# Kernel tuning notes

Measured on AMD Instinct MI355X. Metric: run time of the kernel, lower is better.

The kernel has to match this reference:

```python
import jax, jax.numpy as jnp
import numpy as np

H = 16            # num_heads
D = 64            # head_output_size
DIM = 1024        # model dim (C)
R = 10            # lora rank
ATT_SCALE = D ** -0.5
LORA_SCALE = 1.0 / R   # lora_alpha(=1) / r


def setup_inputs() -> dict:
    key = jax.random.key(0)
    ks = jax.random.split(key, 14)
    B, N = 2, 2048
    s = 0.02
    x = jax.random.normal(ks[0], (B, N, DIM), jnp.float32)
    mask = jax.random.randint(ks[1], (B, N), 0, 2).astype(bool)
    return {
        "x": x,
        "mask": mask,
        "w_qkv": jax.random.normal(ks[2], (3 * H * D, DIM), jnp.float32) * s,
        "wq_base": jax.random.normal(ks[3], (H * D, DIM), jnp.float32) * s,
        "bq_base": jax.random.normal(ks[4], (H * D,), jnp.float32) * s,
        "wq_A": jax.random.normal(ks[5], (R, DIM), jnp.float32) * s,
        "wq_B": jax.random.normal(ks[6], (H * D, R), jnp.float32) * s,
        "wv_base": jax.random.normal(ks[7], (H * D, DIM), jnp.float32) * s,
        "bv_base": jax.random.normal(ks[8], (H * D,), jnp.float32) * s,
        "wv_A": jax.random.normal(ks[9], (R, DIM), jnp.float32) * s,
        "wv_B": jax.random.normal(ks[10], (H * D, R), jnp.float32) * s,
        "w_out": jax.random.normal(ks[11], (DIM, H * D), jnp.float32) * s,
        "b_out": jax.random.normal(ks[12], (DIM,), jnp.float32) * s,
    }


def _lora_linear(x, w_base, b_base, A, Bm):
    # lora.Linear (unmerged): base linear + scaled low-rank path
    return x @ w_base.T + b_base + ((x @ A.T) @ Bm.T) * LORA_SCALE


def reference(x, mask, w_qkv, wq_base, bq_base, wq_A, wq_B,
              wv_base, bv_base, wv_A, wv_B, w_out, b_out):
    B, N, C = x.shape
    # fused qkv projection -> (3, B, H, N, D)
    qkv = (x @ w_qkv.T).reshape(B, N, 3, H, D).transpose(2, 0, 3, 1, 4)
    q, k, v = qkv[0], qkv[1], qkv[2]
    # LoRA-modified q and v, reshaped to (B, H, N, D)
    q_lora = _lora_linear(x, wq_base, bq_base, wq_A, wq_B).reshape(B, N, H, D).transpose(0, 2, 1, 3)
    v_lora = _lora_linear(x, wv_base, bv_base, wv_A, wv_B).reshape(B, N, H, D).transpose(0, 2, 1, 3)
    q = q + q_lora
    v = v + v_lora
    # attention scores (B, H, N, N)
    attn = jnp.einsum('bhnd,bhmd->bhnm', q, k) * ATT_SCALE
    # 2D key-padding mask branch: mask[:, None, None, :]
    attn = jnp.where(mask[:, None, None, :], attn, -jnp.inf)
    attn = jax.nn.softmax(attn, axis=-1)
    out = jnp.einsum('bhnm,bhmd->bhnd', attn, v)
    out = out.transpose(0, 2, 1, 3).reshape(B, N, H * D)  # b h n d -> b n (h d)
    return out @ w_out.T + b_out
```

## Files before the change

### kernel.cpp

```cpp
#include <hip/hip_runtime.h>

typedef unsigned short u16;
typedef unsigned int u32;
typedef __attribute__((ext_vector_type(2))) unsigned int u32x2;
typedef __attribute__((ext_vector_type(4))) unsigned int u32x4;
typedef __attribute__((ext_vector_type(4))) unsigned short u16x4;
typedef __attribute__((ext_vector_type(8))) unsigned short u16x8;
typedef __attribute__((ext_vector_type(8))) short short8;
typedef __attribute__((ext_vector_type(4))) float f32x4;
typedef __attribute__((ext_vector_type(16))) float f32x16;

#define NHEAD 16
#define HDIM 64
#define SEQ 2048
#define MODELD 1024
#define MROWS 4096
#define QKVCOLS 3072
#define QSCALE 0.18033688011112042f

#define WAITVM(N) asm volatile("s_waitcnt vmcnt(" #N ")" ::: "memory")

__device__ __forceinline__ u16 f2bf(float f) {
  union { float f; unsigned u; } v; v.f = f;
  unsigned r = v.u + 0x7FFFu + ((v.u >> 16) & 1u);
  return (u16)(r >> 16);
}

__device__ __forceinline__ u32 cvtpk(float lo, float hi) {
  u32 r;
  asm("v_cvt_pk_bf16_f32 %0, %1, %2" : "=v"(r) : "v"(lo), "v"(hi));
  return r;
}

__device__ __forceinline__ void pl32(u32& a, u32& b) {
  asm("v_permlane32_swap_b32 %0, %1" : "+v"(a), "+v"(b));
}

__device__ __forceinline__ void gload_lds16(const void* g, void* l) {
  __builtin_amdgcn_global_load_lds((const __attribute__((address_space(1))) void*)g,
                                   (__attribute__((address_space(3))) void*)l, 16, 0, 0);
}


__global__ void prep_cast(const float* __restrict__ in, u16* __restrict__ outb) {
  int i = blockIdx.x * 256 + threadIdx.x;
  float4 v = *(const float4*)(in + (size_t)i * 4);
  u16x4 o = {f2bf(v.x), f2bf(v.y), f2bf(v.z), f2bf(v.w)};
  *(u16x4*)(outb + (size_t)i * 4) = o;
}

__global__ void prep_mask(const unsigned int* __restrict__ mraw, u16* __restrict__ mbf) {
  __shared__ int flag;
  const int tid = threadIdx.x;
  if (tid == 0) flag = 0;
  __syncthreads();
  if (mraw[tid] > 1u) flag = 1;
  __syncthreads();
  const int is_bytes = flag;
  const unsigned char* bp = (const unsigned char*)mraw;
  u16x4 o;
#pragma unroll
  for (int j = 0; j < 4; ++j) {
    unsigned v = is_bytes ? (unsigned)bp[tid * 4 + j] : mraw[tid * 4 + j];
    o[j] = v ? (u16)0 : (u16)0xC380;
  }
  *(u16x4*)(mbf + tid * 4) = o;
}

__global__ void prep_w(const float* __restrict__ wqkv,
                       const float* __restrict__ wqb, const float* __restrict__ bq,
                       const float* __restrict__ wqA, const float* __restrict__ wqB,
                       const float* __restrict__ wvb, const float* __restrict__ bv,
                       const float* __restrict__ wvA, const float* __restrict__ wvB,
                       u16* __restrict__ wcomb, float* __restrict__ biasc) {
  const int c = blockIdx.x;
  const int t = c >> 10, hd = c & 1023;
  const int k0 = threadIdx.x * 4;
  float4 w = *(const float4*)(wqkv + (size_t)c * MODELD + k0);
  float a0 = w.x, a1 = w.y, a2 = w.z, a3 = w.w;
  if (t != 1) {
    const float* base = (t == 0 ? wqb : wvb) + (size_t)hd * MODELD + k0;
    const float* A = (t == 0 ? wqA : wvA);
    const float* Bm = (t == 0 ? wqB : wvB) + hd * 10;
    float4 bsv = *(const float4*)base;
    a0 += bsv.x; a1 += bsv.y; a2 += bsv.z; a3 += bsv.w;
#pragma unroll
    for (int j = 0; j < 10; ++j) {
      float bj = Bm[j] * 0.1f;
      float4 av = *(const float4*)(A + (size_t)j * MODELD + k0);
      a0 += bj * av.x; a1 += bj * av.y; a2 += bj * av.z; a3 += bj * av.w;
    }
    if (t == 0) { a0 *= QSCALE; a1 *= QSCALE; a2 *= QSCALE; a3 *= QSCALE; }
  }
  u16x4 o = {f2bf(a0), f2bf(a1), f2bf(a2), f2bf(a3)};
  *(u16x4*)(wcomb + (size_t)c * MODELD + k0) = o;
  if (threadIdx.x == 0)
    biasc[c] = (t == 0) ? QSCALE * bq[hd] : ((t == 2) ? bv[hd] : 0.f);
}

template<int MODE>
__global__ __launch_bounds__(256) void gemm128(const u16* __restrict__ A, const u16* __restrict__ W,
                                               const float* __restrict__ bias,
                                               u16* __restrict__ oq, u16* __restrict__ ok, u16* __restrict__ ov,
                                               float* __restrict__ of) {
  __shared__ __align__(16) char lds[65536];
  const int tid = threadIdx.x;
  const int lane = tid & 63;
  const int wid = tid >> 6;
  const int wr = wid >> 1, wc = wid & 1;
  const int nx = gridDim.x;
  int bid = blockIdx.y * nx + blockIdx.x;
  bid = (bid & 7) * ((nx * gridDim.y) >> 3) + (bid >> 3);
  const int m0 = (bid / nx) << 7;
  const int n0 = (bid % nx) << 7;
  const int K = MODELD;

  f32x4 acc[4][4] = {};
  const int so = wid * 1024 + (lane << 4);

  auto stage = [&](int buf, int kt) {
    char* dst = lds + (buf << 15);
#pragma unroll
    for (int c = 0; c < 4; ++c) {
      const int o = c * 4096 + so;
      const int row = o >> 7;
      const int colb = (o & 127) ^ ((row & 7) << 4);
      gload_lds16((const char*)(A + (size_t)(m0 + row) * K + kt) + colb, dst + (c * 4096 + wid * 1024));
      gload_lds16((const char*)(W + (size_t)(n0 + row) * K + kt) + colb, dst + (16384 + c * 4096 + wid * 1024));
    }
  };

  stage(0, 0);
  __syncthreads();

  for (int t = 0; t < 16; ++t) {
    if (t < 15) stage((t + 1) & 1, (t + 1) << 6);
    const char* base = lds + ((t & 1) << 15);
#pragma unroll
    for (int ks = 0; ks < 2; ++ks) {
      short8 av[4], bv[4];
#pragma unroll
      for (int i = 0; i < 4; ++i) {
        const int arow = wr * 64 + i * 16 + (lane & 15);
        const int off = (ks * 64 + ((lane >> 4) << 4)) ^ ((lane & 7) << 4);
        av[i] = *(const short8*)(base + (arow << 7) + off);
        const int brow = wc * 64 + i * 16 + (lane & 15);
        bv[i] = *(const short8*)(base + 16384 + (brow << 7) + off);
      }
#pragma unroll
      for (int i = 0; i < 4; ++i)
#pragma unroll
        for (int j = 0; j < 4; ++j)
          acc[i][j] = __builtin_amdgcn_mfma_f32_16x16x32_bf16(av[i], bv[j], acc[i][j], 0, 0, 0);
    }
    __syncthreads();
  }

  if (MODE == 0) {
    u16* limg = (u16*)lds;
    const int tsel = n0 >> 10;
    const int hd0 = n0 & 1023;
#pragma unroll
    for (int j = 0; j < 4; ++j) {
      const int cl = wc * 64 + j * 16 + (lane & 15);
      const int head = cl >> 6, d = cl & 63;
      const float bs = bias[n0 + cl];
#pragma unroll
      for (int i = 0; i < 4; ++i) {
        const int kvb = wr * 64 + i * 16 + ((lane >> 4) << 2);
#pragma unroll
        for (int r = 0; r < 4; ++r) {
          const int kvloc = kvb + r;
          const u16 val = f2bf(acc[i][j][r] + bs);
          int off;
          if (tsel == 0) {
            off = head * 8192 + kvloc * 64 + d;
          } else if (tsel == 1) {
            const int kv = kvloc & 63;
            off = head * 8192 + (kvloc >> 6) * 4096 +
                  ((((kv >> 5) & 1) << 2) + (d >> 4)) * 512 +
                  (((kv & 31) + (((d >> 3) & 1) << 5)) << 3) + (d & 7);
          } else {
            const int kv = kvloc & 63;
            off = head * 8192 + (kvloc >> 6) * 4096 +
                  (((d >> 5) << 2) + ((kv >> 4) & 3)) * 512 +
                  (((d & 31) + (((kv >> 3) & 1) << 5)) << 3) + (kv & 7);
          }
          limg[off] = val;
        }
      }
    }
    __syncthreads();
    const int b = m0 >> 11;
#pragma unroll
    for (int p = 0; p < 8; ++p) {
      const int idx = p * 2048 + tid * 8;
      u16x8 v = *(const u16x8*)(limg + idx);
      const int headg = (hd0 >> 6) + (p >> 2);
      const size_t bh = (size_t)(b * NHEAD + headg);
      if (tsel == 0) {
        u16* dst = oq + (bh * SEQ + (m0 & 2047)) * HDIM + (p & 3) * 2048 + tid * 8;
        *(u16x8*)dst = v;
      } else {
        const int tileg = ((m0 & 2047) >> 6) + ((p >> 1) & 1);
        u16* basep = (tsel == 1) ? ok : ov;
        u16* dst = basep + (bh * 32 + tileg) * 4096 + (p & 1) * 2048 + tid * 8;
        *(u16x8*)dst = v;
      }
    }
  } else {
#pragma unroll
    for (int j = 0; j < 4; ++j) {
      const int col = n0 + wc * 64 + j * 16 + (lane & 15);
      const float bs = bias[col];
#pragma unroll
      for (int i = 0; i < 4; ++i) {
        const int rowb = m0 + wr * 64 + i * 16 + ((lane >> 4) << 2);
#pragma unroll
        for (int r = 0; r < 4; ++r)
          of[(size_t)(rowb + r) * MODELD + col] = acc[i][j][r] + bs;
      }
    }
  }
}

__global__ __launch_bounds__(64, 2) void flash_attn(const u16* __restrict__ q, const u16* __restrict__ kfr,
                                                    const u16* __restrict__ vfr, const u16* __restrict__ mbf,
                                                    u16* __restrict__ attnout) {
  const int lane = threadIdx.x;
  const int qi = lane & 31, h = lane >> 5;
  const int bid = blockIdx.x;
  const int xcd = bid & 7, rest = bid >> 3;
  const int bh = xcd * 4 + (rest >> 6);
  const int q0 = (rest & 63) << 5;
  const int b = bh >> 4, hh = bh & 15;

  const int token = q0 + qi;
  short8 qf[4], qf4 = {};
  {
    const u16* qp = q + ((size_t)bh * SEQ + token) * HDIM;
#pragma unroll
    for (int ks = 0; ks < 4; ++ks) qf[ks] = *(const short8*)(qp + ks * 16 + h * 8);
    if (h == 0) qf4[0] = (short)0x3F80;
  }

  const u16* kg = kfr + (size_t)bh * 32 * 4096;
  const u16* vg = vfr + (size_t)bh * 32 * 4096;
  const u16* mrow = mbf + b * SEQ;
  const int lo = lane << 3;

  short8 kS[8], vS[8];
  u16 m0v, m1v;

  f32x16 o0 = {}, o1 = {};
  f32x4 ps = {0.f, 0.f, 0.f, 0.f};

  {
    const u16* kt = kg;
    const u16* vt = vg;
#pragma unroll
    for (int i = 0; i < 8; ++i) kS[i] = *(const short8*)(kt + i * 512 + lo);
#pragma unroll
    for (int i = 0; i < 8; ++i) vS[i] = *(const short8*)(vt + i * 512 + lo);
    m0v = mrow[qi];
    m1v = mrow[32 + qi];
  }

  for (int t = 0; t < 32; ++t) {
    short8 e0 = {}, e1 = {};
    if (h == 0) { e0[0] = (short)m0v; e1[0] = (short)m1v; }

    f32x16 s0 = {}, s1 = {};
    __builtin_amdgcn_s_setprio(1);
#pragma unroll
    for (int ks = 0; ks < 4; ++ks) {
      s0 = __builtin_amdgcn_mfma_f32_32x32x16_bf16(kS[ks], qf[ks], s0, 0, 0, 0);
      s1 = __builtin_amdgcn_mfma_f32_32x32x16_bf16(kS[4 + ks], qf[ks], s1, 0, 0, 0);
    }
    s0 = __builtin_amdgcn_mfma_f32_32x32x16_bf16(e0, qf4, s0, 0, 0, 0);
    s1 = __builtin_amdgcn_mfma_f32_32x32x16_bf16(e1, qf4, s1, 0, 0, 0);
    __builtin_amdgcn_s_setprio(0);

    if (t < 31) {
      const u16* kt = kg + (size_t)(t + 1) * 4096;
#pragma unroll
      for (int i = 0; i < 8; ++i) kS[i] = *(const short8*)(kt + i * 512 + lo);
      m0v = mrow[(t + 1) * 64 + qi];
      m1v = mrow[(t + 1) * 64 + 32 + qi];
    }

    u32 w[16];
#pragma unroll
    for (int blk = 0; blk < 2; ++blk) {
#pragma unroll
      for (int g = 0; g < 4; ++g) {
        float e0f, e1f, e2f, e3f;
        if (blk == 0) {
          e0f = __builtin_amdgcn_exp2f(s0[4 * g + 0]);
          e1f = __builtin_amdgcn_exp2f(s0[4 * g + 1]);
          e2f = __builtin_amdgcn_exp2f(s0[4 * g + 2]);
          e3f = __builtin_amdgcn_exp2f(s0[4 * g + 3]);
        } else {
          e0f = __builtin_amdgcn_exp2f(s1[4 * g + 0]);
          e1f = __builtin_amdgcn_exp2f(s1[4 * g + 1]);
          e2f = __builtin_amdgcn_exp2f(s1[4 * g + 2]);
          e3f = __builtin_amdgcn_exp2f(s1[4 * g + 3]);
        }
        ps[0] += e0f; ps[1] += e1f; ps[2] += e2f; ps[3] += e3f;
        w[blk * 8 + 2 * g] = cvtpk(e0f, e1f);
        w[blk * 8 + 2 * g + 1] = cvtpk(e2f, e3f);
      }
    }
    pl32(w[0], w[2]);  pl32(w[1], w[3]);
    pl32(w[4], w[6]);  pl32(w[5], w[7]);
    pl32(w[8], w[10]); pl32(w[9], w[11]);
    pl32(w[12], w[14]); pl32(w[13], w[15]);

    __builtin_amdgcn_s_setprio(1);
#pragma unroll
    for (int s = 0; s < 4; ++s) {
      u32x4 pw = {w[4 * s], w[4 * s + 1], w[4 * s + 2], w[4 * s + 3]};
      short8 pf = __builtin_bit_cast(short8, pw);
      o0 = __builtin_amdgcn_mfma_f32_32x32x16_bf16(vS[s], pf, o0, 0, 0, 0);
      o1 = __builtin_amdgcn_mfma_f32_32x32x16_bf16(vS[4 + s], pf, o1, 0, 0, 0);
    }
    __builtin_amdgcn_s_setprio(0);

    if (t < 31) {
      const u16* vt = vg + (size_t)(t + 1) * 4096;
#pragma unroll
      for (int i = 0; i < 8; ++i) vS[i] = *(const short8*)(vt + i * 512 + lo);
    }
  }

  float l = (ps[0] + ps[1]) + (ps[2] + ps[3]);
  l += __shfl_xor(l, 32);
  const float inv = 1.0f / l;

  u16* outp = attnout + ((size_t)(b * SEQ + token)) * MODELD + hh * HDIM;
#pragma unroll
  for (int dblk = 0; dblk < 2; ++dblk) {
#pragma unroll
    for (int g = 0; g < 4; ++g) {
      float v0, v1, v2, v3;
      if (dblk == 0) {
        v0 = o0[4 * g + 0]; v1 = o0[4 * g + 1]; v2 = o0[4 * g + 2]; v3 = o0[4 * g + 3];
      } else {
        v0 = o1[4 * g + 0]; v1 = o1[4 * g + 1]; v2 = o1[4 * g + 2]; v3 = o1[4 * g + 3];
      }
      u32x2 ow;
      ow[0] = cvtpk(v0 * inv, v1 * inv);
      ow[1] = cvtpk(v2 * inv, v3 * inv);
      *(u32x2*)(outp + dblk * 32 + g * 8 + h * 4) = ow;
    }
  }
}

extern "C" void kernel_launch(void* const* d_in, const int* in_sizes, int n_in,
                              void* d_out, int out_size, void* d_ws, size_t ws_size,
                              hipStream_t stream) {
  const float* x       = (const float*)d_in[0];
  const unsigned int* mask = (const unsigned int*)d_in[1];
  const float* w_qkv   = (const float*)d_in[2];
  const float* wq_base = (const float*)d_in[3];
  const float* bq      = (const float*)d_in[4];
  const float* wq_A    = (const float*)d_in[5];
  const float* wq_B    = (const float*)d_in[6];
  const float* wv_base = (const float*)d_in[7];
  const float* bv      = (const float*)d_in[8];
  const float* wv_A    = (const float*)d_in[9];
  const float* wv_B    = (const float*)d_in[10];
  const float* w_out   = (const float*)d_in[11];
  const float* b_out   = (const float*)d_in[12];
  float* out = (float*)d_out;

  char* ws = (char*)d_ws;
  u16* xb      = (u16*)(ws);
  u16* wcomb   = (u16*)(ws + 8388608);
  u16* woutb   = (u16*)(ws + 14680064);
  u16* qws     = (u16*)(ws + 16777216);
  u16* kws     = (u16*)(ws + 25165824);
  u16* vws     = (u16*)(ws + 33554432);
  float* biasc = (float*)(ws + 50331648);
  u16* mbf     = (u16*)(ws + 50343936);
  u16* attnout = xb;

  prep_cast<<<4096, 256, 0, stream>>>(x, xb);
  prep_cast<<<1024, 256, 0, stream>>>(w_out, woutb);
  prep_mask<<<1, 1024, 0, stream>>>(mask, mbf);
  prep_w<<<3072, 256, 0, stream>>>(w_qkv, wq_base, bq, wq_A, wq_B,
                                   wv_base, bv, wv_A, wv_B, wcomb, biasc);

  gemm128<0><<<dim3(QKVCOLS / 128, MROWS / 128), 256, 0, stream>>>(
      xb, wcomb, biasc, qws, kws, vws, nullptr);

  flash_attn<<<2048, 64, 0, stream>>>(qws, kws, vws, mbf, attnout);

  gemm128<1><<<dim3(MODELD / 128, MROWS / 128), 256, 0, stream>>>(
      attnout, woutb, b_out, nullptr, nullptr, nullptr, out);
}
```

Measured before the change: 138.8 us.

## Process two 32-query tiles per attention wave to reuse K/V fragments

Each flash-attention wave now handles 64 queries as two 32-query sub-tiles, both sharing the same K and V register fragments loaded once per key block. The grid is halved and the block-to-(head, query) mapping is adjusted to match. This cuts K/V global loads per query in half and gives the second tile's MFMAs time to hide the next K load. In exchange it needs more registers, since the launch-bounds occupancy hint was dropped and four output accumulators are live, and there are fewer waves to spread across CUs.

Result: no change. 137.7 us (-0.8%).

```diff
diff --git a/kernel.cpp b/kernel.cpp
--- a/kernel.cpp
+++ b/kernel.cpp
@@ -17,8 +17,6 @@
 #define MROWS 4096
 #define QKVCOLS 3072
 #define QSCALE 0.18033688011112042f
-
-#define WAITVM(N) asm volatile("s_waitcnt vmcnt(" #N ")" ::: "memory")
 
 __device__ __forceinline__ u16 f2bf(float f) {
   union { float f; unsigned u; } v; v.f = f;
@@ -224,23 +222,26 @@
   }
 }
 
-__global__ __launch_bounds__(64, 2) void flash_attn(const u16* __restrict__ q, const u16* __restrict__ kfr,
-                                                    const u16* __restrict__ vfr, const u16* __restrict__ mbf,
-                                                    u16* __restrict__ attnout) {
+__global__ __launch_bounds__(64) void flash_attn(const u16* __restrict__ q, const u16* __restrict__ kfr,
+                                                 const u16* __restrict__ vfr, const u16* __restrict__ mbf,
+                                                 u16* __restrict__ attnout) {
   const int lane = threadIdx.x;
   const int qi = lane & 31, h = lane >> 5;
   const int bid = blockIdx.x;
   const int xcd = bid & 7, rest = bid >> 3;
-  const int bh = xcd * 4 + (rest >> 6);
-  const int q0 = (rest & 63) << 5;
+  const int bh = xcd * 4 + (rest >> 5);
+  const int q0 = (rest & 31) << 6;
   const int b = bh >> 4, hh = bh & 15;
 
-  const int token = q0 + qi;
-  short8 qf[4], qf4 = {};
+  const int tokenA = q0 + qi;
+  short8 qfA[4], qfB[4], qf4 = {};
   {
-    const u16* qp = q + ((size_t)bh * SEQ + token) * HDIM;
-#pragma unroll
-    for (int ks = 0; ks < 4; ++ks) qf[ks] = *(const short8*)(qp + ks * 16 + h * 8);
+    const u16* qp = q + ((size_t)bh * SEQ + tokenA) * HDIM;
+#pragma unroll
+    for (int ks = 0; ks < 4; ++ks) {
+      qfA[ks] = *(const short8*)(qp + ks * 16 + h * 8);
+      qfB[ks] = *(const short8*)(qp + 32 * HDIM + ks * 16 + h * 8);
+    }
     if (h == 0) qf4[0] = (short)0x3F80;
   }
 
@@ -252,16 +253,14 @@
   short8 kS[8], vS[8];
   u16 m0v, m1v;
 
-  f32x16 o0 = {}, o1 = {};
-  f32x4 ps = {0.f, 0.f, 0.f, 0.f};
+  f32x16 oA0 = {}, oA1 = {}, oB0 = {}, oB1 = {};
+  f32x4 psA = {0.f, 0.f, 0.f, 0.f}, psB = {0.f, 0.f, 0.f, 0.f};
 
   {
-    const u16* kt = kg;
-    const u16* vt = vg;
-#pragma unroll
-    for (int i = 0; i < 8; ++i) kS[i] = *(const short8*)(kt + i * 512 + lo);
-#pragma unroll
-    for (int i = 0; i < 8; ++i) vS[i] = *(const short8*)(vt + i * 512 + lo);
+#pragma unroll
+    for (int i = 0; i < 8; ++i) kS[i] = *(const short8*)(kg + i * 512 + lo);
+#pragma unroll
+    for (int i = 0; i < 8; ++i) vS[i] = *(const short8*)(vg + i * 512 + lo);
     m0v = mrow[qi];
     m1v = mrow[32 + qi];
   }
@@ -274,20 +273,12 @@
     __builtin_amdgcn_s_setprio(1);
 #pragma unroll
     for (int ks = 0; ks < 4; ++ks) {
-      s0 = __builtin_amdgcn_mfma_f32_32x32x16_bf16(kS[ks], qf[ks], s0, 0, 0, 0);
-      s1 = __builtin_amdgcn_mfma_f32_32x32x16_bf16(kS[4 + ks], qf[ks], s1, 0, 0, 0);
+      s0 = __builtin_amdgcn_mfma_f32_32x32x16_bf16(kS[ks], qfA[ks], s0, 0, 0, 0);
+      s1 = __builtin_amdgcn_mfma_f32_32x32x16_bf16(kS[4 + ks], qfA[ks], s1, 0, 0, 0);
     }
     s0 = __builtin_amdgcn_mfma_f32_32x32x16_bf16(e0, qf4, s0, 0, 0, 0);
     s1 = __builtin_amdgcn_mfma_f32_32x32x16_bf16(e1, qf4, s1, 0, 0, 0);
     __builtin_amdgcn_s_setprio(0);
-
-    if (t < 31) {
-      const u16* kt = kg + (size_t)(t + 1) * 4096;
-#pragma unroll
-      for (int i = 0; i < 8; ++i) kS[i] = *(const short8*)(kt + i * 512 + lo);
-      m0v = mrow[(t + 1) * 64 + qi];
-      m1v = mrow[(t + 1) * 64 + 32 + qi];
-    }
 
     u32 w[16];
 #pragma unroll
@@ -306,7 +297,7 @@
           e2f = __builtin_amdgcn_exp2f(s1[4 * g + 2]);
           e3f = __builtin_amdgcn_exp2f(s1[4 * g + 3]);
         }
-        ps[0] += e0f; ps[1] += e1f; ps[2] += e2f; ps[3] += e3f;
+        psA[0] += e0f; psA[1] += e1f; psA[2] += e2f; psA[3] += e3f;
         w[blk * 8 + 2 * g] = cvtpk(e0f, e1f);
         w[blk * 8 + 2 * g + 1] = cvtpk(e2f, e3f);
       }
@@ -321,8 +312,61 @@
     for (int s = 0; s < 4; ++s) {
       u32x4 pw = {w[4 * s], w[4 * s + 1], w[4 * s + 2], w[4 * s + 3]};
       short8 pf = __builtin_bit_cast(short8, pw);
-      o0 = __builtin_amdgcn_mfma_f32_32x32x16_bf16(vS[s], pf, o0, 0, 0, 0);
-      o1 = __builtin_amdgcn_mfma_f32_32x32x16_bf16(vS[4 + s], pf, o1, 0, 0, 0);
+      oA0 = __builtin_amdgcn_mfma_f32_32x32x16_bf16(vS[s], pf, oA0, 0, 0, 0);
+      oA1 = __builtin_amdgcn_mfma_f32_32x32x16_bf16(vS[4 + s], pf, oA1, 0, 0, 0);
+    }
+
+    f32x16 r0 = {}, r1 = {};
+#pragma unroll
+    for (int ks = 0; ks < 4; ++ks) {
+      r0 = __builtin_amdgcn_mfma_f32_32x32x16_bf16(kS[ks], qfB[ks], r0, 0, 0, 0);
+      r1 = __builtin_amdgcn_mfma_f32_32x32x16_bf16(kS[4 + ks], qfB[ks], r1, 0, 0, 0);
+    }
+    r0 = __builtin_amdgcn_mfma_f32_32x32x16_bf16(e0, qf4, r0, 0, 0, 0);
+    r1 = __builtin_amdgcn_mfma_f32_32x32x16_bf16(e1, qf4, r1, 0, 0, 0);
+    __builtin_amdgcn_s_setprio(0);
+
+    if (t < 31) {
+      const u16* kt = kg + (size_t)(t + 1) * 4096;
+#pragma unroll
+      for (int i = 0; i < 8; ++i) kS[i] = *(const short8*)(kt + i * 512 + lo);
+      m0v = mrow[(t + 1) * 64 + qi];
+      m1v = mrow[(t + 1) * 64 + 32 + qi];
+    }
+
+#pragma unroll
+    for (int blk = 0; blk < 2; ++blk) {
+#pragma unroll
+      for (int g = 0; g < 4; ++g) {
+        float e0f, e1f, e2f, e3f;
+        if (blk == 0) {
+          e0f = __builtin_amdgcn_exp2f(r0[4 * g + 0]);
+          e1f = __builtin_amdgcn_exp2f(r0[4 * g + 1]);
+          e2f = __builtin_amdgcn_exp2f(r0[4 * g + 2]);
+          e3f = __builtin_amdgcn_exp2f(r0[4 * g + 3]);
+        } else {
+          e0f = __builtin_amdgcn_exp2f(r1[4 * g + 0]);
+          e1f = __builtin_amdgcn_exp2f(r1[4 * g + 1]);
+          e2f = __builtin_amdgcn_exp2f(r1[4 * g + 2]);
+          e3f = __builtin_amdgcn_exp2f(r1[4 * g + 3]);
+        }
+        psB[0] += e0f; psB[1] += e1f; psB[2] += e2f; psB[3] += e3f;
+        w[blk * 8 + 2 * g] = cvtpk(e0f, e1f);
+        w[blk * 8 + 2 * g + 1] = cvtpk(e2f, e3f);
+      }
+    }
+    pl32(w[0], w[2]);  pl32(w[1], w[3]);
+    pl32(w[4], w[6]);  pl32(w[5], w[7]);
+    pl32(w[8], w[10]); pl32(w[9], w[11]);
+    pl32(w[12], w[14]); pl32(w[13], w[15]);
+
+    __builtin_amdgcn_s_setprio(1);
+#pragma unroll
+    for (int s = 0; s < 4; ++s) {
+      u32x4 pw = {w[4 * s], w[4 * s + 1], w[4 * s + 2], w[4 * s + 3]};
+      short8 pf = __builtin_bit_cast(short8, pw);
+      oB0 = __builtin_amdgcn_mfma_f32_32x32x16_bf16(vS[s], pf, oB0, 0, 0, 0);
+      oB1 = __builtin_amdgcn_mfma_f32_32x32x16_bf16(vS[4 + s], pf, oB1, 0, 0, 0);
     }
     __builtin_amdgcn_s_setprio(0);
 
@@ -333,25 +377,33 @@
     }
   }
 
-  float l = (ps[0] + ps[1]) + (ps[2] + ps[3]);
-  l += __shfl_xor(l, 32);
-  const float inv = 1.0f / l;
-
-  u16* outp = attnout + ((size_t)(b * SEQ + token)) * MODELD + hh * HDIM;
+  float lA = (psA[0] + psA[1]) + (psA[2] + psA[3]);
+  lA += __shfl_xor(lA, 32);
+  float lB = (psB[0] + psB[1]) + (psB[2] + psB[3]);
+  lB += __shfl_xor(lB, 32);
+  const float invA = 1.0f / lA, invB = 1.0f / lB;
+
+  u16* outp = attnout + ((size_t)(b * SEQ + tokenA)) * MODELD + hh * HDIM;
 #pragma unroll
   for (int dblk = 0; dblk < 2; ++dblk) {
 #pragma unroll
     for (int g = 0; g < 4; ++g) {
-      float v0, v1, v2, v3;
+      float a0, a1, a2, a3, b0, b1, b2, b3;
       if (dblk == 0) {
-        v0 = o0[4 * g + 0]; v1 = o0[4 * g + 1]; v2 = o0[4 * g + 2]; v3 = o0[4 * g + 3];
+        a0 = oA0[4 * g + 0]; a1 = oA0[4 * g + 1]; a2 = oA0[4 * g + 2]; a3 = oA0[4 * g + 3];
+        b0 = oB0[4 * g + 0]; b1 = oB0[4 * g + 1]; b2 = oB0[4 * g + 2]; b3 = oB0[4 * g + 3];
       } else {
-        v0 = o1[4 * g + 0]; v1 = o1[4 * g + 1]; v2 = o1[4 * g + 2]; v3 = o1[4 * g + 3];
+        a0 = oA1[4 * g + 0]; a1 = oA1[4 * g + 1]; a2 = oA1[4 * g + 2]; a3 = oA1[4 * g + 3];
+        b0 = oB1[4 * g + 0]; b1 = oB1[4 * g + 1]; b2 = oB1[4 * g + 2]; b3 = oB1[4 * g + 3];
       }
       u32x2 ow;
-      ow[0] = cvtpk(v0 * inv, v1 * inv);
-      ow[1] = cvtpk(v2 * inv, v3 * inv);
+      ow[0] = cvtpk(a0 * invA, a1 * invA);
+      ow[1] = cvtpk(a2 * invA, a3 * invA);
       *(u32x2*)(outp + dblk * 32 + g * 8 + h * 4) = ow;
+      u32x2 ob;
+      ob[0] = cvtpk(b0 * invB, b1 * invB);
+      ob[1] = cvtpk(b2 * invB, b3 * invB);
+      *(u32x2*)(outp + 32 * MODELD + dblk * 32 + g * 8 + h * 4) = ob;
     }
   }
 }
@@ -394,7 +446,7 @@
   gemm128<0><<<dim3(QKVCOLS / 128, MROWS / 128), 256, 0, stream>>>(
       xb, wcomb, biasc, qws, kws, vws, nullptr);
 
-  flash_attn<<<2048, 64, 0, stream>>>(qws, kws, vws, mbf, attnout);
+  flash_attn<<<1024, 64, 0, stream>>>(qws, kws, vws, mbf, attnout);
 
   gemm128<1><<<dim3(MODELD / 128, MROWS / 128), 256, 0, stream>>>(
       attnout, woutb, b_out, nullptr, nullptr, nullptr, out);
```

## Split attention key range across two waves and merge partial outputs in LDS

Applied to the files above, without the earlier changes.

The flash attention kernel now launches two waves per block, and each wave processes half of the key/value tiles for the same 32 queries. The partial output accumulators and row sums are written to shared memory, combined after a block barrier, normalized, and stored. This doubles the number of active waves to improve latency hiding, since the kernel previously ran one wave per block with a long serial loop. The cost is extra LDS traffic, a __syncthreads, and a final reduction step. The launch bounds change to 128 threads and 4 blocks per CU.

New measurement: 252.9 us. +82.2%, slower.

```diff
diff --git a/kernel.cpp b/kernel.cpp
--- a/kernel.cpp
+++ b/kernel.cpp
@@ -17,8 +17,6 @@
 #define MROWS 4096
 #define QKVCOLS 3072
 #define QSCALE 0.18033688011112042f
-
-#define WAITVM(N) asm volatile("s_waitcnt vmcnt(" #N ")" ::: "memory")
 
 __device__ __forceinline__ u16 f2bf(float f) {
   union { float f; unsigned u; } v; v.f = f;
@@ -224,10 +222,13 @@
   }
 }
 
-__global__ __launch_bounds__(64, 2) void flash_attn(const u16* __restrict__ q, const u16* __restrict__ kfr,
-                                                    const u16* __restrict__ vfr, const u16* __restrict__ mbf,
-                                                    u16* __restrict__ attnout) {
-  const int lane = threadIdx.x;
+__global__ __launch_bounds__(128, 4) void flash_attn(const u16* __restrict__ q, const u16* __restrict__ kfr,
+                                                     const u16* __restrict__ vfr, const u16* __restrict__ mbf,
+                                                     u16* __restrict__ attnout) {
+  __shared__ __align__(16) float oL[2][2][4][64][4];
+  __shared__ float lL[2][32];
+  const int tid = threadIdx.x;
+  const int lane = tid & 63, wid = tid >> 6;
   const int qi = lane & 31, h = lane >> 5;
   const int bid = blockIdx.x;
   const int xcd = bid & 7, rest = bid >> 3;
@@ -248,6 +249,7 @@
   const u16* vg = vfr + (size_t)bh * 32 * 4096;
   const u16* mrow = mbf + b * SEQ;
   const int lo = lane << 3;
+  const int t0 = wid << 4;
 
   short8 kS[8], vS[8];
   u16 m0v, m1v;
@@ -256,17 +258,18 @@
   f32x4 ps = {0.f, 0.f, 0.f, 0.f};
 
   {
-    const u16* kt = kg;
-    const u16* vt = vg;
+    const u16* kt = kg + (size_t)t0 * 4096;
+    const u16* vt = vg + (size_t)t0 * 4096;
 #pragma unroll
     for (int i = 0; i < 8; ++i) kS[i] = *(const short8*)(kt + i * 512 + lo);
 #pragma unroll
     for (int i = 0; i < 8; ++i) vS[i] = *(const short8*)(vt + i * 512 + lo);
-    m0v = mrow[qi];
-    m1v = mrow[32 + qi];
-  }
-
-  for (int t = 0; t < 32; ++t) {
+    m0v = mrow[t0 * 64 + qi];
+    m1v = mrow[t0 * 64 + 32 + qi];
+  }
+
+  for (int tt = 0; tt < 16; ++tt) {
+    const int t = t0 + tt;
     short8 e0 = {}, e1 = {};
     if (h == 0) { e0[0] = (short)m0v; e1[0] = (short)m1v; }
 
@@ -281,7 +284,7 @@
     s1 = __builtin_amdgcn_mfma_f32_32x32x16_bf16(e1, qf4, s1, 0, 0, 0);
     __builtin_amdgcn_s_setprio(0);
 
-    if (t < 31) {
+    if (tt < 15) {
       const u16* kt = kg + (size_t)(t + 1) * 4096;
 #pragma unroll
       for (int i = 0; i < 8; ++i) kS[i] = *(const short8*)(kt + i * 512 + lo);
@@ -326,7 +329,7 @@
     }
     __builtin_amdgcn_s_setprio(0);
 
-    if (t < 31) {
+    if (tt < 15) {
       const u16* vt = vg + (size_t)(t + 1) * 4096;
 #pragma unroll
       for (int i = 0; i < 8; ++i) vS[i] = *(const short8*)(vt + i * 512 + lo);
@@ -335,24 +338,25 @@
 
   float l = (ps[0] + ps[1]) + (ps[2] + ps[3]);
   l += __shfl_xor(l, 32);
-  const float inv = 1.0f / l;
-
-  u16* outp = attnout + ((size_t)(b * SEQ + token)) * MODELD + hh * HDIM;
-#pragma unroll
-  for (int dblk = 0; dblk < 2; ++dblk) {
-#pragma unroll
-    for (int g = 0; g < 4; ++g) {
-      float v0, v1, v2, v3;
-      if (dblk == 0) {
-        v0 = o0[4 * g + 0]; v1 = o0[4 * g + 1]; v2 = o0[4 * g + 2]; v3 = o0[4 * g + 3];
-      } else {
-        v0 = o1[4 * g + 0]; v1 = o1[4 * g + 1]; v2 = o1[4 * g + 2]; v3 = o1[4 * g + 3];
-      }
-      u32x2 ow;
-      ow[0] = cvtpk(v0 * inv, v1 * inv);
-      ow[1] = cvtpk(v2 * inv, v3 * inv);
-      *(u32x2*)(outp + dblk * 32 + g * 8 + h * 4) = ow;
-    }
+  if (h == 0) lL[wid][qi] = l;
+
+#pragma unroll
+  for (int c = 0; c < 4; ++c) {
+    *(f32x4*)&oL[wid][0][c][lane][0] = f32x4{o0[4 * c], o0[4 * c + 1], o0[4 * c + 2], o0[4 * c + 3]};
+    *(f32x4*)&oL[wid][1][c][lane][0] = f32x4{o1[4 * c], o1[4 * c + 1], o1[4 * c + 2], o1[4 * c + 3]};
+  }
+  __syncthreads();
+
+  const float inv = 1.0f / (lL[0][qi] + lL[1][qi]);
+  u16* outp = attnout + ((size_t)(b * SEQ + token)) * MODELD + hh * HDIM + wid * 32;
+#pragma unroll
+  for (int g = 0; g < 4; ++g) {
+    f32x4 pa = *(const f32x4*)&oL[0][wid][g][lane][0];
+    f32x4 pb = *(const f32x4*)&oL[1][wid][g][lane][0];
+    u32x2 ow;
+    ow[0] = cvtpk((pa[0] + pb[0]) * inv, (pa[1] + pb[1]) * inv);
+    ow[1] = cvtpk((pa[2] + pb[2]) * inv, (pa[3] + pb[3]) * inv);
+    *(u32x2*)(outp + g * 8 + h * 4) = ow;
   }
 }
 
@@ -394,7 +398,7 @@
   gemm128<0><<<dim3(QKVCOLS / 128, MROWS / 128), 256, 0, stream>>>(
       xb, wcomb, biasc, qws, kws, vws, nullptr);
 
-  flash_attn<<<2048, 64, 0, stream>>>(qws, kws, vws, mbf, attnout);
+  flash_attn<<<2048, 128, 0, stream>>>(qws, kws, vws, mbf, attnout);
 
   gemm128<1><<<dim3(MODELD / 128, MROWS / 128), 256, 0, stream>>>(
       attnout, woutb, b_out, nullptr, nullptr, nullptr, out);
```
